# Optimization experiments

Hardware: AMD Instinct MI355X
Metric: run time of the kernel (lower is better)

Reference implementation:

```python
import jax, jax.numpy as jnp
import numpy as np

B, S, H, F, E, K = 2, 2048, 1024, 2048, 8, 2  # batch, seq, hidden, ffn, experts, top_k


def setup_inputs() -> dict:
    key = jax.random.key(0)
    k1, k2, k3, k4 = jax.random.split(key, 4)
    s = lambda n: 1.0 / np.sqrt(n)
    return {
        "x": jax.random.normal(k1, (B, S, H), jnp.float32),
        "w_router": jax.random.normal(k2, (H, E), jnp.float32) * s(H),
        "w_in": jax.random.normal(k3, (E, H, 2 * F), jnp.float32) * s(H),   # GLU: 2*ffn
        "w_out": jax.random.normal(k4, (E, F, H), jnp.float32) * s(F),
        "bias": jnp.zeros((H,), jnp.float32),
    }


def reference(x, w_router, w_in, w_out, bias):
    Bq, Sq, Hq = x.shape
    T = Bq * Sq
    xf = x.reshape(T, Hq)

    # --- TopKGating ---
    logits = xf @ w_router                       # [T, E]
    top_vals, top_idx = jax.lax.top_k(logits, K)  # [T, K]
    gates = jax.nn.softmax(top_vals, axis=-1)    # softmax over selected logits

    # JetMoE-style aux loss: switch loss + 0.1 * z-loss
    probs = jax.nn.softmax(logits, axis=-1)
    p = probs.sum(0); p = p / p.sum()
    freq = jnp.sum(jax.nn.one_hot(top_idx, E, dtype=logits.dtype), axis=(0, 1))
    f = freq / freq.sum()
    lsesq = jnp.sum(jax.nn.logsumexp(logits, axis=-1) ** 2)
    loss = E * jnp.sum(p * f) + 0.1 * lsesq / T

    # --- dispatch: one row per (token, selected expert) pair, token-major ---
    eid = top_idx.reshape(-1)                    # [T*K] expert id per row
    g = gates.reshape(-1)                        # [T*K] gate per row
    tok = jnp.repeat(jnp.arange(T), K)           # [T*K] source token per row
    xr = jnp.repeat(xf, K, axis=0)               # [T*K, H]

    # --- grouped expert GEMMs (masked per-expert; math-equivalent to grouped GEMM) ---
    out_rows = jnp.zeros((T * K, Hq), x.dtype)
    for e in range(E):
        sel = (eid == e).astype(x.dtype)[:, None]
        h = (xr * sel) @ w_in[e]                 # [T*K, 2F]
        a, gv = jnp.split(h, 2, axis=-1)
        h = jax.nn.silu(a) * gv                  # GLU
        out_rows = out_rows + sel * (h @ w_out[e])

    # --- combine: scale by gates, scatter-add back to tokens ---
    out_rows = out_rows * g[:, None]
    y = jax.ops.segment_sum(out_rows, tok, num_segments=T)
    y = y.reshape(Bq, Sq, Hq) + bias
    return y, loss
```

## Files before the change

### kernel.cpp

```cpp
#include <hip/hip_runtime.h>
#include <hip/hip_bf16.h>
#include <math.h>

#define T_TOK 4096
#define HDIM  1024
#define FDIM  2048
#define EDIM  8
#define KSEL  2
#define TKROW 8192
#define N2F   4096
#define MAX_SLOTS 72

typedef __attribute__((ext_vector_type(8))) short short8;
typedef __attribute__((ext_vector_type(4))) float f32x4;

__device__ __forceinline__ unsigned short f32_to_bf16(float f) {
  unsigned int u = __float_as_uint(f);
  u += 0x7FFFu + ((u >> 16) & 1u);
  return (unsigned short)(u >> 16);
}

__device__ __forceinline__ void gload16(const void* g, void* l) {
  __builtin_amdgcn_global_load_lds(
      (const __attribute__((address_space(1))) unsigned int*)g,
      (__attribute__((address_space(3))) unsigned int*)l, 16, 0, 0);
}


__global__ void transpose_conv_kernel(const float* __restrict__ in,
                                      unsigned short* __restrict__ out,
                                      int R, int C) {
  __shared__ float tile[64][65];
  long base = (long)blockIdx.z * (long)R * (long)C;
  int c0 = blockIdx.x * 64, r0 = blockIdx.y * 64;
  int tx = threadIdx.x & 63;
  int ty = threadIdx.x >> 6;
  #pragma unroll
  for (int j = 0; j < 64; j += 4) {
    int r = r0 + ty + j;
    tile[ty + j][tx] = in[base + (long)r * C + c0 + tx];
  }
  __syncthreads();
  int ow = threadIdx.x & 31;
  int ocg = threadIdx.x >> 5;
  #pragma unroll
  for (int j = 0; j < 64; j += 8) {
    int oc = ocg + j;
    ushort2 o;
    o.x = f32_to_bf16(tile[2 * ow][oc]);
    o.y = f32_to_bf16(tile[2 * ow + 1][oc]);
    *(ushort2*)(out + base + (long)(c0 + oc) * R + r0 + 2 * ow) = o;
  }
}

__global__ void router_kernel(const float* __restrict__ x,
                              const float* __restrict__ wr,
                              unsigned short* __restrict__ xbout,
                              int* __restrict__ eid, float* __restrict__ tgate,
                              float* __restrict__ p_sum,
                              float* __restrict__ lse2_sum,
                              int* __restrict__ counts) {
  __shared__ float s_p[EDIM];
  __shared__ float s_lse2;
  __shared__ int s_cnt[EDIM];
  if (threadIdx.x < EDIM) { s_p[threadIdx.x] = 0.f; s_cnt[threadIdx.x] = 0; }
  if (threadIdx.x == 0) s_lse2 = 0.f;
  __syncthreads();

  int wave = threadIdx.x >> 6;
  int lane = threadIdx.x & 63;

  for (int it = 0; it < 4; ++it) {
    int t = (blockIdx.x * 4 + wave) + it * 1024;
    float acc[EDIM];
    #pragma unroll
    for (int e = 0; e < EDIM; e++) acc[e] = 0.f;
    const float* xr = x + (long)t * HDIM;
    unsigned short* xo = xbout + (long)t * HDIM;
    #pragma unroll
    for (int c = 0; c < 4; ++c) {
      int h0 = lane * 4 + c * 256;
      float4 v = *(const float4*)(xr + h0);
      ushort4 o;
      o.x = f32_to_bf16(v.x); o.y = f32_to_bf16(v.y);
      o.z = f32_to_bf16(v.z); o.w = f32_to_bf16(v.w);
      *(ushort4*)(xo + h0) = o;
      const float* w0 = wr + (long)h0 * EDIM;
      #pragma unroll
      for (int e = 0; e < EDIM; e++)
        acc[e] += v.x * w0[e] + v.y * w0[EDIM + e] +
                  v.z * w0[2 * EDIM + e] + v.w * w0[3 * EDIM + e];
    }
    #pragma unroll
    for (int e = 0; e < EDIM; e++) {
      float v = acc[e];
      for (int off = 32; off > 0; off >>= 1) v += __shfl_down(v, off);
      acc[e] = v;
    }
    if (lane == 0) {
      float m = acc[0];
      #pragma unroll
      for (int e = 1; e < EDIM; e++) m = fmaxf(m, acc[e]);
      float ex[EDIM]; float se = 0.f;
      #pragma unroll
      for (int e = 0; e < EDIM; e++) { ex[e] = __expf(acc[e] - m); se += ex[e]; }
      float lse = m + __logf(se);
      atomicAdd(&s_lse2, lse * lse);
      float inv = 1.f / se;
      #pragma unroll
      for (int e = 0; e < EDIM; e++) atomicAdd(&s_p[e], ex[e] * inv);
      int i1 = 0;
      #pragma unroll
      for (int e = 1; e < EDIM; e++) if (acc[e] > acc[i1]) i1 = e;
      int i2 = (i1 == 0) ? 1 : 0;
      #pragma unroll
      for (int e = 0; e < EDIM; e++) if (e != i1 && acc[e] > acc[i2]) i2 = e;
      float g1 = 1.f / (1.f + __expf(acc[i2] - acc[i1]));
      eid[t * 2] = i1; eid[t * 2 + 1] = i2;
      tgate[t * 2] = g1; tgate[t * 2 + 1] = 1.f - g1;
      atomicAdd(&s_cnt[i1], 1); atomicAdd(&s_cnt[i2], 1);
    }
  }
  __syncthreads();
  if (threadIdx.x < EDIM) {
    atomicAdd(&p_sum[threadIdx.x], s_p[threadIdx.x]);
    atomicAdd(&counts[threadIdx.x], s_cnt[threadIdx.x]);
  }
  if (threadIdx.x == 0) atomicAdd(lse2_sum, s_lse2);
}

__global__ void scan_kernel(const int* __restrict__ counts,
                            int* __restrict__ offsets, int* __restrict__ slot_e,
                            int* __restrict__ slot_m0, int* __restrict__ slot_rows,
                            int* __restrict__ n_slots, int* __restrict__ cursors) {
  int off = 0, s = 0;
  for (int e = 0; e < EDIM; e++) {
    offsets[e] = off;
    cursors[e] = 0;
    int c = counts[e];
    for (int m0 = 0; m0 < c; m0 += 128) {
      slot_e[s] = e; slot_m0[s] = off + m0;
      slot_rows[s] = min(128, c - m0); s++;
    }
    off += c;
  }
  *n_slots = s;
}

__global__ void scatter_kernel(const int* __restrict__ eid,
                               const float* __restrict__ tgate,
                               const int* __restrict__ offsets,
                               int* __restrict__ cursors,
                               int* __restrict__ btok, float* __restrict__ bgate,
                               int* __restrict__ tpos) {
  __shared__ int lcnt[EDIM];
  __shared__ int lbase[EDIM];
  int tid = threadIdx.x;
  if (tid < EDIM) lcnt[tid] = 0;
  __syncthreads();
  int t = blockIdx.x * 256 + tid;
  int e0 = eid[t * 2], e1 = eid[t * 2 + 1];
  int p0 = atomicAdd(&lcnt[e0], 1);
  int p1 = atomicAdd(&lcnt[e1], 1);
  __syncthreads();
  if (tid < EDIM) lbase[tid] = atomicAdd(&cursors[tid], lcnt[tid]);
  __syncthreads();
  int r0 = offsets[e0] + lbase[e0] + p0;
  int r1 = offsets[e1] + lbase[e1] + p1;
  btok[r0] = t; bgate[r0] = tgate[t * 2];     tpos[t * 2] = r0;
  btok[r1] = t; bgate[r1] = tgate[t * 2 + 1]; tpos[t * 2 + 1] = r1;
}

__global__ __launch_bounds__(256) void gemm1_kernel(
    const unsigned short* __restrict__ xb,
    const unsigned short* __restrict__ w_inT,
    const int* __restrict__ btok,
    const int* __restrict__ slot_e, const int* __restrict__ slot_m0,
    const int* __restrict__ slot_rows, const int* __restrict__ n_slots,
    unsigned short* __restrict__ glu)
{
  int bx = blockIdx.x;
  int slot = (bx & 7) * 9 + (bx >> 3);
  if (slot >= *n_slots) return;
  int e = slot_e[slot], r0 = slot_m0[slot], nrows = slot_rows[slot];
  int by = blockIdx.y;

  __shared__ unsigned short lA[128 * 64];
  __shared__ unsigned short lB[256 * 64];

  int tid = threadIdx.x;
  int lane = tid & 63, wv = tid >> 6;
  int wr = wv >> 1, wc = wv & 1;
  int lm = lane & 15, lq = lane >> 4, l7 = lane & 7;

  int srow = tid >> 3, skc = tid & 7;
  const unsigned short* asrc[4];
  const unsigned short* bsrc[8];
  #pragma unroll
  for (int i = 0; i < 4; ++i) {
    int row = srow + i * 32;
    int swz = (skc ^ (row & 7)) * 8;
    int ar = min(row, nrows - 1);
    int tok = btok[r0 + ar];
    asrc[i] = xb + (long)tok * HDIM + swz;
  }
  #pragma unroll
  for (int i = 0; i < 8; ++i) {
    int row = srow + i * 32;
    int swz = (skc ^ (row & 7)) * 8;
    int w = row >> 7, r = row & 127;
    int bcol = (r < 64) ? (by * 128 + w * 64 + r)
                        : (FDIM + by * 128 + w * 64 + (r - 64));
    bsrc[i] = w_inT + ((long)e * N2F + bcol) * HDIM + swz;
  }

  f32x4 acc[4][8];
  #pragma unroll
  for (int mf = 0; mf < 4; ++mf)
    #pragma unroll
    for (int nf = 0; nf < 8; ++nf) acc[mf][nf] = (f32x4){0.f, 0.f, 0.f, 0.f};

  for (int k0 = 0; k0 < HDIM; k0 += 64) {
    #pragma unroll
    for (int i = 0; i < 4; ++i) gload16(asrc[i] + k0, &lA[tid * 8 + i * 2048]);
    #pragma unroll
    for (int i = 0; i < 8; ++i) gload16(bsrc[i] + k0, &lB[tid * 8 + i * 2048]);
    __syncthreads();
    #pragma unroll
    for (int ks = 0; ks < 2; ++ks) {
      short8 a[4];
      #pragma unroll
      for (int mf = 0; mf < 4; ++mf) {
        int row = wr * 64 + mf * 16 + lm;
        a[mf] = *(const short8*)&lA[row * 64 + (((ks * 4 + lq) ^ l7) * 8)];
      }
      #pragma unroll
      for (int nf = 0; nf < 8; ++nf) {
        int n = wc * 128 + nf * 16 + lm;
        short8 b = *(const short8*)&lB[n * 64 + (((ks * 4 + lq) ^ l7) * 8)];
        #pragma unroll
        for (int mf = 0; mf < 4; ++mf)
          acc[mf][nf] = __builtin_amdgcn_mfma_f32_16x16x32_bf16(a[mf], b, acc[mf][nf], 0, 0, 0);
      }
    }
    __syncthreads();
  }

  #pragma unroll
  for (int mf = 0; mf < 4; ++mf) {
    #pragma unroll
    for (int r = 0; r < 4; ++r) {
      int row = wr * 64 + mf * 16 + lq * 4 + r;
      if (row < nrows) {
        #pragma unroll
        for (int nf = 0; nf < 4; ++nf) {
          float a = acc[mf][nf][r];
          float g = acc[mf][nf + 4][r];
          float val = (a / (1.f + __expf(-a))) * g;
          glu[(long)(r0 + row) * FDIM + by * 128 + wc * 64 + nf * 16 + lm] = f32_to_bf16(val);
        }
      }
    }
  }
}

__global__ __launch_bounds__(256) void gemm2_kernel(
    const unsigned short* __restrict__ glu,
    const unsigned short* __restrict__ w_outT,
    const float* __restrict__ bgate,
    const int* __restrict__ slot_e, const int* __restrict__ slot_m0,
    const int* __restrict__ slot_rows, const int* __restrict__ n_slots,
    float* __restrict__ orows)
{
  int bx = blockIdx.x;
  int slot = (bx & 7) * 9 + (bx >> 3);
  if (slot >= *n_slots) return;
  int e = slot_e[slot], r0 = slot_m0[slot], nrows = slot_rows[slot];
  int c0 = blockIdx.y * 128;

  __shared__ unsigned short lA[128 * 64];
  __shared__ unsigned short lB[128 * 64];

  int tid = threadIdx.x;
  int lane = tid & 63, wv = tid >> 6;
  int wr = wv >> 1, wc = wv & 1;
  int lm = lane & 15, lq = lane >> 4, l7 = lane & 7;

  int srow = tid >> 3, skc = tid & 7;
  const unsigned short* asrc[4];
  const unsigned short* bsrc[4];
  #pragma unroll
  for (int i = 0; i < 4; ++i) {
    int row = srow + i * 32;
    int swz = (skc ^ (row & 7)) * 8;
    int ar = min(row, nrows - 1);
    asrc[i] = glu + (long)(r0 + ar) * FDIM + swz;
    bsrc[i] = w_outT + ((long)e * HDIM + c0 + row) * FDIM + swz;
  }

  f32x4 acc[4][4];
  #pragma unroll
  for (int mf = 0; mf < 4; ++mf)
    #pragma unroll
    for (int nf = 0; nf < 4; ++nf) acc[mf][nf] = (f32x4){0.f, 0.f, 0.f, 0.f};

  for (int k0 = 0; k0 < FDIM; k0 += 64) {
    #pragma unroll
    for (int i = 0; i < 4; ++i) {
      gload16(asrc[i] + k0, &lA[tid * 8 + i * 2048]);
      gload16(bsrc[i] + k0, &lB[tid * 8 + i * 2048]);
    }
    __syncthreads();
    #pragma unroll
    for (int ks = 0; ks < 2; ++ks) {
      short8 a[4], b[4];
      #pragma unroll
      for (int mf = 0; mf < 4; ++mf) {
        int row = wr * 64 + mf * 16 + lm;
        a[mf] = *(const short8*)&lA[row * 64 + (((ks * 4 + lq) ^ l7) * 8)];
      }
      #pragma unroll
      for (int nf = 0; nf < 4; ++nf) {
        int n = wc * 64 + nf * 16 + lm;
        b[nf] = *(const short8*)&lB[n * 64 + (((ks * 4 + lq) ^ l7) * 8)];
      }
      #pragma unroll
      for (int mf = 0; mf < 4; ++mf)
        #pragma unroll
        for (int nf = 0; nf < 4; ++nf)
          acc[mf][nf] = __builtin_amdgcn_mfma_f32_16x16x32_bf16(a[mf], b[nf], acc[mf][nf], 0, 0, 0);
    }
    __syncthreads();
  }

  #pragma unroll
  for (int mf = 0; mf < 4; ++mf) {
    #pragma unroll
    for (int r = 0; r < 4; ++r) {
      int row = wr * 64 + mf * 16 + lq * 4 + r;
      if (row < nrows) {
        float g = bgate[r0 + row];
        #pragma unroll
        for (int nf = 0; nf < 4; ++nf) {
          orows[(long)(r0 + row) * HDIM + c0 + wc * 64 + nf * 16 + lm] = acc[mf][nf][r] * g;
        }
      }
    }
  }
}

__global__ void combine_kernel(const float* __restrict__ orows,
                               const int* __restrict__ tpos,
                               const float* __restrict__ bias,
                               float* __restrict__ y) {
  int i = blockIdx.x * 256 + threadIdx.x;
  int t = i >> 8;
  int h = (i & 255) * 4;
  int p0 = tpos[t * 2], p1 = tpos[t * 2 + 1];
  float4 a = *(const float4*)(orows + (long)p0 * HDIM + h);
  float4 b = *(const float4*)(orows + (long)p1 * HDIM + h);
  float4 bv = *(const float4*)(bias + h);
  float4 o;
  o.x = a.x + b.x + bv.x; o.y = a.y + b.y + bv.y;
  o.z = a.z + b.z + bv.z; o.w = a.w + b.w + bv.w;
  *(float4*)(y + (long)t * HDIM + h) = o;
}

__global__ void finalize_kernel(const float* __restrict__ p_sum,
                                const float* __restrict__ lse2,
                                const int* __restrict__ counts,
                                float* __restrict__ loss_out) {
  float P = 0.f;
  for (int e = 0; e < EDIM; e++) P += p_sum[e];
  float dot = 0.f;
  for (int e = 0; e < EDIM; e++)
    dot += (p_sum[e] / P) * ((float)counts[e] / (float)TKROW);
  *loss_out = (float)EDIM * dot + 0.1f * (*lse2) / (float)T_TOK;
}

extern "C" void kernel_launch(void* const* d_in, const int* in_sizes, int n_in,
                              void* d_out, int out_size, void* d_ws, size_t ws_size,
                              hipStream_t stream) {
  const float* x        = (const float*)d_in[0];
  const float* w_router = (const float*)d_in[1];
  const float* w_in     = (const float*)d_in[2];
  const float* w_out    = (const float*)d_in[3];
  const float* bias     = (const float*)d_in[4];
  float* y = (float*)d_out;

  char* ws = (char*)d_ws;
  size_t o = 0;
  auto alloc = [&](size_t bytes) { size_t r = o; o = (o + bytes + 255) & ~(size_t)255; return r; };
  size_t o_meta    = alloc(256);
  size_t o_offsets = alloc(EDIM * 4);
  size_t o_slot_e  = alloc(MAX_SLOTS * 4);
  size_t o_slot_m0 = alloc(MAX_SLOTS * 4);
  size_t o_slot_nr = alloc(MAX_SLOTS * 4);
  size_t o_eid     = alloc((size_t)T_TOK * 2 * 4);
  size_t o_tgate   = alloc((size_t)T_TOK * 2 * 4);
  size_t o_tpos    = alloc((size_t)T_TOK * 2 * 4);
  size_t o_btok    = alloc((size_t)TKROW * 4);
  size_t o_bgate   = alloc((size_t)TKROW * 4);
  size_t o_xb      = alloc((size_t)T_TOK * HDIM * 2);
  size_t o_winT    = alloc((size_t)EDIM * N2F * HDIM * 2);
  size_t o_woutT   = alloc((size_t)EDIM * HDIM * FDIM * 2);
  size_t o_glu     = alloc((size_t)TKROW * FDIM * 2);
  size_t o_orows   = o_winT;
  (void)ws_size;

  float* p_sum   = (float*)(ws + o_meta);
  float* lse2    = (float*)(ws + o_meta + 32);
  int*   counts  = (int*)(ws + o_meta + 64);
  int*   cursors = (int*)(ws + o_meta + 96);
  int*   n_slots = (int*)(ws + o_meta + 128);
  int*   offsets = (int*)(ws + o_offsets);
  int*   slot_e  = (int*)(ws + o_slot_e);
  int*   slot_m0 = (int*)(ws + o_slot_m0);
  int*   slot_nr = (int*)(ws + o_slot_nr);
  int*   eid     = (int*)(ws + o_eid);
  float* tgate   = (float*)(ws + o_tgate);
  int*   tpos    = (int*)(ws + o_tpos);
  int*   btok    = (int*)(ws + o_btok);
  float* bgate   = (float*)(ws + o_bgate);
  unsigned short* xb    = (unsigned short*)(ws + o_xb);
  unsigned short* winT  = (unsigned short*)(ws + o_winT);
  unsigned short* woutT = (unsigned short*)(ws + o_woutT);
  unsigned short* glu   = (unsigned short*)(ws + o_glu);
  float* orows = (float*)(ws + o_orows);

  hipMemsetAsync(ws, 0, 256, stream);

  transpose_conv_kernel<<<dim3(N2F / 64, HDIM / 64, EDIM), dim3(256), 0, stream>>>(
      w_in, winT, HDIM, N2F);
  transpose_conv_kernel<<<dim3(HDIM / 64, FDIM / 64, EDIM), dim3(256), 0, stream>>>(
      w_out, woutT, FDIM, HDIM);

  router_kernel<<<dim3(256), dim3(256), 0, stream>>>(
      x, w_router, xb, eid, tgate, p_sum, lse2, counts);
  scan_kernel<<<dim3(1), dim3(1), 0, stream>>>(
      counts, offsets, slot_e, slot_m0, slot_nr, n_slots, cursors);
  scatter_kernel<<<dim3(T_TOK / 256), dim3(256), 0, stream>>>(
      eid, tgate, offsets, cursors, btok, bgate, tpos);

  gemm1_kernel<<<dim3(MAX_SLOTS, FDIM / 128), dim3(256), 0, stream>>>(
      xb, winT, btok, slot_e, slot_m0, slot_nr, n_slots, glu);
  gemm2_kernel<<<dim3(MAX_SLOTS, HDIM / 128), dim3(256), 0, stream>>>(
      glu, woutT, bgate, slot_e, slot_m0, slot_nr, n_slots, orows);

  combine_kernel<<<dim3((T_TOK * HDIM) / 1024), dim3(256), 0, stream>>>(
      orows, tpos, bias, y);
  finalize_kernel<<<dim3(1), dim3(1), 0, stream>>>(
      p_sum, lse2, counts, y + (size_t)T_TOK * HDIM);
}
```

Measured before the change: 559.8 us.

## Double-buffer LDS in expert GEMMs and shrink gemm1 N-tile to 128

Both grouped expert GEMM kernels now use two LDS buffers, so the global-to-LDS load for the next K step is issued before computing the current one. This overlaps memory latency with MFMA work and removes one barrier per iteration. gemm1's tile shrinks from 128x256 to 128x128 (64 GLU output columns per block), which halves accumulator registers and doubles the grid in the F dimension. In exchange, the x rows are reloaded more often and per-block arithmetic intensity drops.

Result: faster. 533.3 us (-4.7%).

```diff
diff --git a/kernel.cpp b/kernel.cpp
--- a/kernel.cpp
+++ b/kernel.cpp
@@ -185,8 +185,8 @@
   int e = slot_e[slot], r0 = slot_m0[slot], nrows = slot_rows[slot];
   int by = blockIdx.y;
 
-  __shared__ unsigned short lA[128 * 64];
-  __shared__ unsigned short lB[256 * 64];
+  __shared__ unsigned short lA[2][128 * 64];
+  __shared__ unsigned short lB[2][128 * 64];
 
   int tid = threadIdx.x;
   int lane = tid & 63, wv = tid >> 6;
@@ -195,7 +195,7 @@
 
   int srow = tid >> 3, skc = tid & 7;
   const unsigned short* asrc[4];
-  const unsigned short* bsrc[8];
+  const unsigned short* bsrc[4];
   #pragma unroll
   for (int i = 0; i < 4; ++i) {
     int row = srow + i * 32;
@@ -203,46 +203,55 @@
     int ar = min(row, nrows - 1);
     int tok = btok[r0 + ar];
     asrc[i] = xb + (long)tok * HDIM + swz;
-  }
-  #pragma unroll
-  for (int i = 0; i < 8; ++i) {
-    int row = srow + i * 32;
-    int swz = (skc ^ (row & 7)) * 8;
-    int w = row >> 7, r = row & 127;
-    int bcol = (r < 64) ? (by * 128 + w * 64 + r)
-                        : (FDIM + by * 128 + w * 64 + (r - 64));
+    int group = row >> 5, within = row & 31;
+    int bcol = by * 64 + (group >> 1) * 32 + within + ((group & 1) ? FDIM : 0);
     bsrc[i] = w_inT + ((long)e * N2F + bcol) * HDIM + swz;
   }
 
-  f32x4 acc[4][8];
+  f32x4 acc[4][4];
   #pragma unroll
   for (int mf = 0; mf < 4; ++mf)
     #pragma unroll
-    for (int nf = 0; nf < 8; ++nf) acc[mf][nf] = (f32x4){0.f, 0.f, 0.f, 0.f};
-
-  for (int k0 = 0; k0 < HDIM; k0 += 64) {
-    #pragma unroll
-    for (int i = 0; i < 4; ++i) gload16(asrc[i] + k0, &lA[tid * 8 + i * 2048]);
-    #pragma unroll
-    for (int i = 0; i < 8; ++i) gload16(bsrc[i] + k0, &lB[tid * 8 + i * 2048]);
-    __syncthreads();
+    for (int nf = 0; nf < 4; ++nf) acc[mf][nf] = (f32x4){0.f, 0.f, 0.f, 0.f};
+
+  auto stage = [&](unsigned short* dA, unsigned short* dB, int k0) {
+    #pragma unroll
+    for (int i = 0; i < 4; ++i) {
+      gload16(asrc[i] + k0, dA + tid * 8 + i * 2048);
+      gload16(bsrc[i] + k0, dB + tid * 8 + i * 2048);
+    }
+  };
+  auto compute = [&](const unsigned short* cA, const unsigned short* cB) {
     #pragma unroll
     for (int ks = 0; ks < 2; ++ks) {
-      short8 a[4];
+      short8 a[4], b[4];
       #pragma unroll
       for (int mf = 0; mf < 4; ++mf) {
         int row = wr * 64 + mf * 16 + lm;
-        a[mf] = *(const short8*)&lA[row * 64 + (((ks * 4 + lq) ^ l7) * 8)];
-      }
-      #pragma unroll
-      for (int nf = 0; nf < 8; ++nf) {
-        int n = wc * 128 + nf * 16 + lm;
-        short8 b = *(const short8*)&lB[n * 64 + (((ks * 4 + lq) ^ l7) * 8)];
+        a[mf] = *(const short8*)&cA[row * 64 + (((ks * 4 + lq) ^ l7) * 8)];
+      }
+      #pragma unroll
+      for (int nf = 0; nf < 4; ++nf) {
+        int n = wc * 64 + nf * 16 + lm;
+        b[nf] = *(const short8*)&cB[n * 64 + (((ks * 4 + lq) ^ l7) * 8)];
+      }
+      #pragma unroll
+      for (int mf = 0; mf < 4; ++mf)
         #pragma unroll
-        for (int mf = 0; mf < 4; ++mf)
-          acc[mf][nf] = __builtin_amdgcn_mfma_f32_16x16x32_bf16(a[mf], b, acc[mf][nf], 0, 0, 0);
-      }
-    }
+        for (int nf = 0; nf < 4; ++nf)
+          acc[mf][nf] = __builtin_amdgcn_mfma_f32_16x16x32_bf16(a[mf], b[nf], acc[mf][nf], 0, 0, 0);
+    }
+  };
+
+  stage(&lA[0][0], &lB[0][0], 0);
+  __syncthreads();
+  const int NIT = HDIM / 64;
+  for (int it = 0; it < NIT; it += 2) {
+    if (it + 1 < NIT) stage(&lA[1][0], &lB[1][0], (it + 1) * 64);
+    compute(&lA[0][0], &lB[0][0]);
+    __syncthreads();
+    if (it + 2 < NIT) stage(&lA[0][0], &lB[0][0], (it + 2) * 64);
+    compute(&lA[1][0], &lB[1][0]);
     __syncthreads();
   }
 
@@ -253,11 +262,11 @@
       int row = wr * 64 + mf * 16 + lq * 4 + r;
       if (row < nrows) {
         #pragma unroll
-        for (int nf = 0; nf < 4; ++nf) {
+        for (int nf = 0; nf < 2; ++nf) {
           float a = acc[mf][nf][r];
-          float g = acc[mf][nf + 4][r];
+          float g = acc[mf][nf + 2][r];
           float val = (a / (1.f + __expf(-a))) * g;
-          glu[(long)(r0 + row) * FDIM + by * 128 + wc * 64 + nf * 16 + lm] = f32_to_bf16(val);
+          glu[(long)(r0 + row) * FDIM + by * 64 + wc * 32 + nf * 16 + lm] = f32_to_bf16(val);
         }
       }
     }
@@ -278,8 +287,8 @@
   int e = slot_e[slot], r0 = slot_m0[slot], nrows = slot_rows[slot];
   int c0 = blockIdx.y * 128;
 
-  __shared__ unsigned short lA[128 * 64];
-  __shared__ unsigned short lB[128 * 64];
+  __shared__ unsigned short lA[2][128 * 64];
+  __shared__ unsigned short lB[2][128 * 64];
 
   int tid = threadIdx.x;
   int lane = tid & 63, wv = tid >> 6;
@@ -304,25 +313,26 @@
     #pragma unroll
     for (int nf = 0; nf < 4; ++nf) acc[mf][nf] = (f32x4){0.f, 0.f, 0.f, 0.f};
 
-  for (int k0 = 0; k0 < FDIM; k0 += 64) {
+  auto stage = [&](unsigned short* dA, unsigned short* dB, int k0) {
     #pragma unroll
     for (int i = 0; i < 4; ++i) {
-      gload16(asrc[i] + k0, &lA[tid * 8 + i * 2048]);
-      gload16(bsrc[i] + k0, &lB[tid * 8 + i * 2048]);
-    }
-    __syncthreads();
+      gload16(asrc[i] + k0, dA + tid * 8 + i * 2048);
+      gload16(bsrc[i] + k0, dB + tid * 8 + i * 2048);
+    }
+  };
+  auto compute = [&](const unsigned short* cA, const unsigned short* cB) {
     #pragma unroll
     for (int ks = 0; ks < 2; ++ks) {
       short8 a[4], b[4];
       #pragma unroll
       for (int mf = 0; mf < 4; ++mf) {
         int row = wr * 64 + mf * 16 + lm;
-        a[mf] = *(const short8*)&lA[row * 64 + (((ks * 4 + lq) ^ l7) * 8)];
+        a[mf] = *(const short8*)&cA[row * 64 + (((ks * 4 + lq) ^ l7) * 8)];
       }
       #pragma unroll
       for (int nf = 0; nf < 4; ++nf) {
         int n = wc * 64 + nf * 16 + lm;
-        b[nf] = *(const short8*)&lB[n * 64 + (((ks * 4 + lq) ^ l7) * 8)];
+        b[nf] = *(const short8*)&cB[n * 64 + (((ks * 4 + lq) ^ l7) * 8)];
       }
       #pragma unroll
       for (int mf = 0; mf < 4; ++mf)
@@ -330,6 +340,17 @@
         for (int nf = 0; nf < 4; ++nf)
           acc[mf][nf] = __builtin_amdgcn_mfma_f32_16x16x32_bf16(a[mf], b[nf], acc[mf][nf], 0, 0, 0);
     }
+  };
+
+  stage(&lA[0][0], &lB[0][0], 0);
+  __syncthreads();
+  const int NIT = FDIM / 64;
+  for (int it = 0; it < NIT; it += 2) {
+    if (it + 1 < NIT) stage(&lA[1][0], &lB[1][0], (it + 1) * 64);
+    compute(&lA[0][0], &lB[0][0]);
+    __syncthreads();
+    if (it + 2 < NIT) stage(&lA[0][0], &lB[0][0], (it + 2) * 64);
+    compute(&lA[1][0], &lB[1][0]);
     __syncthreads();
   }
 
@@ -442,7 +463,7 @@
   scatter_kernel<<<dim3(T_TOK / 256), dim3(256), 0, stream>>>(
       eid, tgate, offsets, cursors, btok, bgate, tpos);
 
-  gemm1_kernel<<<dim3(MAX_SLOTS, FDIM / 128), dim3(256), 0, stream>>>(
+  gemm1_kernel<<<dim3(MAX_SLOTS, FDIM / 64), dim3(256), 0, stream>>>(
       xb, winT, btok, slot_e, slot_m0, slot_nr, n_slots, glu);
   gemm2_kernel<<<dim3(MAX_SLOTS, HDIM / 128), dim3(256), 0, stream>>>(
       glu, woutT, bgate, slot_e, slot_m0, slot_nr, n_slots, orows);
```
